# Kernel optimization log

Measured on AMD Instinct MI355X. Metric: run time of the kernel, lower is better.

The kernel has to match this reference:

```python
import jax, jax.numpy as jnp
import numpy as np

B, T, F, U, H = 4096, 64, 128, 256, 256
MC_STEPS = 32
DENOISE = True


def setup_inputs() -> dict:
    key = jax.random.key(0)
    ks = jax.random.split(key, 12)
    su = 1.0 / np.sqrt(U)
    inp = {
        "x": jax.random.normal(ks[0], (B, T, F), jnp.float32),
        # LSTM params (torch gate order i,f,g,o)
        "W_ih": jax.random.uniform(ks[1], (4 * U, F), jnp.float32, -su, su),
        "W_hh": jax.random.uniform(ks[2], (4 * U, U), jnp.float32, -su, su),
        "b_ih": jax.random.uniform(ks[3], (4 * U,), jnp.float32, -su, su),
        "b_hh": jax.random.uniform(ks[4], (4 * U,), jnp.float32, -su, su),
        # CRBM conditioning nets: bias (ny), precision (ny), weights (ny*nh)
        "bias_W": jax.random.normal(ks[5], (F, U), jnp.float32) * su,
        "bias_b": jnp.zeros((F,), jnp.float32),
        "prec_W": jax.random.normal(ks[6], (F, U), jnp.float32) * su,
        "prec_b": jnp.zeros((F,), jnp.float32),
        "wts_W": jax.random.normal(ks[7], (F * H, U), jnp.float32) * su,
        "wts_b": jnp.zeros((F * H,), jnp.float32),
    }
    return inp


def _lstm_last_hidden(x, W_ih, W_hh, b_ih, b_hh):
    # single-layer batch_first LSTM; returns last hidden state [B, U]
    b, u = x.shape[0], W_hh.shape[1]
    bias = b_ih + b_hh

    def step(carry, xt):
        h, c = carry
        g = xt @ W_ih.T + h @ W_hh.T + bias          # [B, 4U]
        i, f, gg, o = jnp.split(g, 4, axis=-1)
        c = jax.nn.sigmoid(f) * c + jax.nn.sigmoid(i) * jnp.tanh(gg)
        h = jax.nn.sigmoid(o) * jnp.tanh(c)
        return (h, c), None

    h0 = jnp.zeros((b, u), x.dtype)
    (h, _), _ = jax.lax.scan(step, (h0, h0), jnp.swapaxes(x, 0, 1))
    return h


def _crbm_sample(xh, bias_W, bias_b, prec_W, prec_b, wts_W, wts_b,
                 mc_steps=MC_STEPS, denoise=DENOISE):
    b = xh.shape[0]
    bias = xh @ bias_W.T + bias_b                              # [B, F]
    precision = jax.nn.softplus(xh @ prec_W.T + prec_b) + 1e-6  # [B, F] > 0
    weights = (xh @ wts_W.T + wts_b).reshape(b, F, H)           # [B, F, H]
    std = jax.lax.rsqrt(precision)

    key = jax.random.key(1)
    k0, kloop = jax.random.split(key)
    y0 = bias + std * jax.random.normal(k0, bias.shape, bias.dtype)

    def gibbs(y, k):
        kh, ky = jax.random.split(k)
        h_prob = jax.nn.sigmoid(jnp.einsum("bf,bfh->bh", y, weights))
        h = (jax.random.uniform(kh, h_prob.shape) < h_prob).astype(y.dtype)
        mean = bias + jnp.einsum("bfh,bh->bf", weights, h) / precision
        y = mean + std * jax.random.normal(ky, mean.shape, mean.dtype)
        return y, mean

    y_last, means = jax.lax.scan(gibbs, y0, jax.random.split(kloop, mc_steps))
    y_model = means[-1] if denoise else y_last
    return y_model, bias, precision, weights


def reference(x, W_ih, W_hh, b_ih, b_hh, bias_W, bias_b, prec_W, prec_b, wts_W, wts_b):
    xh = _lstm_last_hidden(x, W_ih, W_hh, b_ih, b_hh)
    y_model, _, _, _ = _crbm_sample(xh, bias_W, bias_b, prec_W, prec_b, wts_W, wts_b)
    return y_model
```

## Files before the change

kernel.cpp:

```cpp
#include <hip/hip_runtime.h>
#include <stdint.h>

#pragma clang fp contract(off)

#define B 4096
#define T 64
#define F 128
#define U 256
#define H 256
#define GU 1024
#define NJ 32768
#define MC 32
#define CH 256
#define BT 32

__host__ __device__ inline void tf2x32(uint32_t k0, uint32_t k1,
                                       uint32_t x0, uint32_t x1,
                                       uint32_t& o0, uint32_t& o1) {
  uint32_t ks2 = k0 ^ k1 ^ 0x1BD11BDAu;
  x0 += k0; x1 += k1;
#define TFR(r) { x0 += x1; x1 = (x1 << r) | (x1 >> (32 - r)); x1 ^= x0; }
  TFR(13) TFR(15) TFR(26) TFR(6)
  x0 += k1;  x1 += ks2 + 1u;
  TFR(17) TFR(29) TFR(16) TFR(24)
  x0 += ks2; x1 += k0 + 2u;
  TFR(13) TFR(15) TFR(26) TFR(6)
  x0 += k0;  x1 += k1 + 3u;
  TFR(17) TFR(29) TFR(16) TFR(24)
  x0 += k1;  x1 += ks2 + 4u;
  TFR(13) TFR(15) TFR(26) TFR(6)
  x0 += ks2; x1 += k0 + 5u;
#undef TFR
  o0 = x0; o1 = x1;
}

__device__ inline uint32_t tf_bits(uint32_t kx, uint32_t ky, uint32_t i) {
  uint32_t o0, o1;
  tf2x32(kx, ky, 0u, i, o0, o1);
  return o0 ^ o1;
}

__device__ inline float u01_f32(uint32_t bits) {
  return __uint_as_float((bits >> 9) | 0x3F800000u) - 1.0f;
}

__device__ inline float erfinv_f32(float x) {
  float w = -log1pf(-(x * x));
  float p;
  if (w < 5.0f) {
    float ww = w - 2.5f;
    p = 2.81022636e-08f;
    p = p * ww + 3.43273939e-07f;
    p = p * ww + (-3.5233877e-06f);
    p = p * ww + (-4.39150654e-06f);
    p = p * ww + 0.00021858087f;
    p = p * ww + (-0.00125372503f);
    p = p * ww + (-0.00417768164f);
    p = p * ww + 0.246640727f;
    p = p * ww + 1.50140941f;
  } else {
    float ww = sqrtf(w) - 3.0f;
    p = -0.000200214257f;
    p = p * ww + 0.000100950558f;
    p = p * ww + 0.00134934322f;
    p = p * ww + (-0.00367342844f);
    p = p * ww + 0.00573950773f;
    p = p * ww + (-0.0076224613f);
    p = p * ww + 0.00943887047f;
    p = p * ww + 1.00167406f;
    p = p * ww + 2.83297682f;
  }
  return p * x;
}

__device__ inline float normal_f32(uint32_t kx, uint32_t ky, uint32_t i) {
  float f = u01_f32(tf_bits(kx, ky, i));
  const float lo = -0.99999994039535522461f;
  float v = f * 2.0f + lo;
  v = fmaxf(lo, v);
  return 1.4142135623730951f * erfinv_f32(v);
}

__device__ inline float sigmoid_f32(float x) {
  return 1.0f / (1.0f + expf(-x));
}
__device__ inline float softplus_f32(float x) {
  return fmaxf(x, 0.0f) + log1pf(expf(-fabsf(x)));
}

__global__ void prep_lstm_w_k(const float* __restrict__ W_ih, const float* __restrict__ W_hh,
                              const float* __restrict__ b_ih, const float* __restrict__ b_hh,
                              float4* __restrict__ w4t, float* __restrict__ biasg) {
  int idx = blockIdx.x * 256 + threadIdx.x;
  if (idx < GU * 96) {
    int j = idx / 96, k4 = idx - j * 96;
    float v[4];
#pragma unroll
    for (int m = 0; m < 4; ++m) {
      int k = k4 * 4 + m;
      v[m] = (k < F) ? W_ih[(size_t)j * F + k] : W_hh[(size_t)j * U + (k - F)];
    }
    w4t[(size_t)k4 * GU + j] = make_float4(v[0], v[1], v[2], v[3]);
  }
  if (idx < GU) biasg[idx] = b_ih[idx] + b_hh[idx];
}

__global__ void prep_wts_k(const float* __restrict__ wts_W, float4* __restrict__ wts4t) {
  int idx = blockIdx.x * 256 + threadIdx.x;
  if (idx >= NJ * 64) return;
  int j = idx >> 6, k4 = idx & 63;
  const float* r = wts_W + (size_t)j * U + k4 * 4;
  wts4t[(size_t)k4 * NJ + j] = make_float4(r[0], r[1], r[2], r[3]);
}

__global__ void prep_bp_k(const float* __restrict__ bias_W, const float* __restrict__ prec_W,
                          float4* __restrict__ bp4t) {
  int idx = blockIdx.x * 256 + threadIdx.x;
  if (idx >= 256 * 64) return;
  int j = idx >> 6, k4 = idx & 63;
  const float* r = (j < F) ? (bias_W + (size_t)j * U + k4 * 4)
                           : (prec_W + (size_t)(j - F) * U + k4 * 4);
  bp4t[(size_t)k4 * 256 + j] = make_float4(r[0], r[1], r[2], r[3]);
}

__global__ __launch_bounds__(256) void lstm_step_k(
    const float* __restrict__ x, const float* __restrict__ h_in,
    const float* __restrict__ c_in, const float4* __restrict__ w4t,
    const float* __restrict__ biasg, float* __restrict__ h_out,
    float* __restrict__ c_out, int t) {
  __shared__ __align__(16) float xt[BT * 128];
  __shared__ __align__(16) float ht[BT * 256];
  const int tid = threadIdx.x;
  const int b0 = blockIdx.x * BT;
  const int ut = blockIdx.y;
  for (int q = tid; q < BT * 32; q += 256) {
    int row = q >> 5, c4 = q & 31;
    *(float4*)(xt + row * 128 + c4 * 4) =
        *(const float4*)(x + ((size_t)(b0 + row) * T + t) * F + c4 * 4);
  }
  for (int q = tid; q < BT * 64; q += 256) {
    int row = q >> 6, c4 = q & 63;
    *(float4*)(ht + row * 256 + c4 * 4) =
        *(const float4*)(h_in + (size_t)(b0 + row) * U + c4 * 4);
  }
  __syncthreads();
  const int u_loc = tid & 63, bg = tid >> 6;
  const int u = ut * 64 + u_loc;
  float accX[4][8], accH[4][8];
#pragma unroll
  for (int g = 0; g < 4; ++g)
#pragma unroll
    for (int b = 0; b < 8; ++b) { accX[g][b] = 0.0f; accH[g][b] = 0.0f; }

#pragma unroll 4
  for (int k4 = 0; k4 < 32; ++k4) {
    float4 wf[4];
#pragma unroll
    for (int g = 0; g < 4; ++g) wf[g] = w4t[(size_t)k4 * GU + g * U + u];
#pragma unroll
    for (int b = 0; b < 8; ++b) {
      float4 av = *(const float4*)(xt + (bg * 8 + b) * 128 + k4 * 4);
#pragma unroll
      for (int g = 0; g < 4; ++g) {
        accX[g][b] = fmaf(av.x, wf[g].x, accX[g][b]);
        accX[g][b] = fmaf(av.y, wf[g].y, accX[g][b]);
        accX[g][b] = fmaf(av.z, wf[g].z, accX[g][b]);
        accX[g][b] = fmaf(av.w, wf[g].w, accX[g][b]);
      }
    }
  }
#pragma unroll 4
  for (int k4 = 32; k4 < 96; ++k4) {
    float4 wf[4];
#pragma unroll
    for (int g = 0; g < 4; ++g) wf[g] = w4t[(size_t)k4 * GU + g * U + u];
#pragma unroll
    for (int b = 0; b < 8; ++b) {
      float4 av = *(const float4*)(ht + (bg * 8 + b) * 256 + (k4 - 32) * 4);
#pragma unroll
      for (int g = 0; g < 4; ++g) {
        accH[g][b] = fmaf(av.x, wf[g].x, accH[g][b]);
        accH[g][b] = fmaf(av.y, wf[g].y, accH[g][b]);
        accH[g][b] = fmaf(av.z, wf[g].z, accH[g][b]);
        accH[g][b] = fmaf(av.w, wf[g].w, accH[g][b]);
      }
    }
  }
  float bi = biasg[u], bf = biasg[U + u], bgg = biasg[2 * U + u], bo = biasg[3 * U + u];
#pragma unroll
  for (int b = 0; b < 8; ++b) {
    size_t gi = (size_t)(b0 + bg * 8 + b) * U + u;
    float c = c_in[gi];
    float g_i = (accX[0][b] + accH[0][b]) + bi;
    float g_f = (accX[1][b] + accH[1][b]) + bf;
    float g_g = (accX[2][b] + accH[2][b]) + bgg;
    float g_o = (accX[3][b] + accH[3][b]) + bo;
    float t1 = sigmoid_f32(g_f) * c;
    float t2 = sigmoid_f32(g_i) * tanhf(g_g);
    float cn = t1 + t2;
    float hn = sigmoid_f32(g_o) * tanhf(cn);
    c_out[gi] = cn;
    h_out[gi] = hn;
  }
}

__global__ __launch_bounds__(256) void gemm_xh_k(
    const float* __restrict__ xh_c, const float4* __restrict__ wts4t,
    const float* __restrict__ wts_b, float* __restrict__ outp) {
  __shared__ __align__(16) float xl[64 * 256];
  const int tid = threadIdx.x;
  const int b0 = blockIdx.x * 64;
  const int j = blockIdx.y * 256 + tid;
  for (int q = tid; q < 64 * 64; q += 256) {
    int row = q >> 6, c4 = q & 63;
    *(float4*)(xl + row * 256 + c4 * 4) =
        *(const float4*)(xh_c + (size_t)(b0 + row) * U + c4 * 4);
  }
  __syncthreads();
  float acc[64];
#pragma unroll
  for (int b = 0; b < 64; ++b) acc[b] = 0.0f;
  for (int k4 = 0; k4 < 64; ++k4) {
    float4 wf = wts4t[(size_t)k4 * NJ + j];
#pragma unroll
    for (int b = 0; b < 64; ++b) {
      float4 av = *(const float4*)(xl + b * 256 + k4 * 4);
      acc[b] = fmaf(av.x, wf.x, acc[b]);
      acc[b] = fmaf(av.y, wf.y, acc[b]);
      acc[b] = fmaf(av.z, wf.z, acc[b]);
      acc[b] = fmaf(av.w, wf.w, acc[b]);
    }
  }
  float bb = wts_b[j];
#pragma unroll
  for (int b = 0; b < 64; ++b)
    outp[(size_t)(b0 + b) * NJ + j] = acc[b] + bb;
}

__global__ __launch_bounds__(256) void biasprec_k(
    const float* __restrict__ xh, const float4* __restrict__ bp4t,
    const float* __restrict__ bias_b, const float* __restrict__ prec_b,
    float* __restrict__ bias_g, float* __restrict__ prec_g) {
  __shared__ __align__(16) float xl[64 * 256];
  const int tid = threadIdx.x;
  const int b0 = blockIdx.x * 64;
  const int j = tid;
  for (int q = tid; q < 64 * 64; q += 256) {
    int row = q >> 6, c4 = q & 63;
    *(float4*)(xl + row * 256 + c4 * 4) =
        *(const float4*)(xh + (size_t)(b0 + row) * U + c4 * 4);
  }
  __syncthreads();
  float acc[64];
#pragma unroll
  for (int b = 0; b < 64; ++b) acc[b] = 0.0f;
  for (int k4 = 0; k4 < 64; ++k4) {
    float4 wf = bp4t[(size_t)k4 * 256 + j];
#pragma unroll
    for (int b = 0; b < 64; ++b) {
      float4 av = *(const float4*)(xl + b * 256 + k4 * 4);
      acc[b] = fmaf(av.x, wf.x, acc[b]);
      acc[b] = fmaf(av.y, wf.y, acc[b]);
      acc[b] = fmaf(av.z, wf.z, acc[b]);
      acc[b] = fmaf(av.w, wf.w, acc[b]);
    }
  }
  if (j < F) {
    float bb = bias_b[j];
#pragma unroll
    for (int b = 0; b < 64; ++b)
      bias_g[(size_t)(b0 + b) * F + j] = acc[b] + bb;
  } else {
    float pb = prec_b[j - F];
#pragma unroll
    for (int b = 0; b < 64; ++b)
      prec_g[(size_t)(b0 + b) * F + (j - F)] = softplus_f32(acc[b] + pb) + 1e-6f;
  }
}

struct GKeys {
  uint32_t k0x, k0y;
  uint32_t khx[32], khy[32], kyx[32], kyy[32];
};

__global__ __launch_bounds__(256) void gibbs_k(
    const float* __restrict__ w_g, const float* __restrict__ bias_g,
    const float* __restrict__ prec_g, float* __restrict__ outp, GKeys keys,
    int base) {
  __shared__ __align__(16) float wl[32768];
  __shared__ __align__(16) float yv[128];
  __shared__ __align__(16) float hv[256];
  __shared__ float bs[128];
  __shared__ float ps[128];
  __shared__ float ss[128];
  const int tid = threadIdx.x;
  const int bloc = blockIdx.x;
  const int gb = base + bloc;
  const float4* src = (const float4*)(w_g + (size_t)bloc * NJ);
  float4* wl4 = (float4*)wl;
  for (int q = tid; q < NJ / 4; q += 256) {
    int f = q >> 6;
    int j4 = q & 63;
    wl4[f * 64 + (j4 ^ (f & 7))] = src[q];
  }
  if (tid < F) {
    float bb = bias_g[(size_t)gb * F + tid];
    float pp = prec_g[(size_t)gb * F + tid];
    bs[tid] = bb; ps[tid] = pp;
    float sd = 1.0f / sqrtf(pp);
    ss[tid] = sd;
    float n = normal_f32(keys.k0x, keys.k0y, (uint32_t)(gb * F + tid));
    float t1 = sd * n;
    yv[tid] = bb + t1;
  }
  __syncthreads();
  for (int s_ = 0; s_ < MC; ++s_) {
    {
      const int j = tid;
      const int jq = j >> 2, jm = j & 3;
      float u = u01_f32(tf_bits(keys.khx[s_], keys.khy[s_], (uint32_t)(gb * H + j)));
      float acc = 0.0f;
#pragma unroll 4
      for (int fb = 0; fb < F; fb += 4) {
        float4 y4 = *(const float4*)(yv + fb);
        float w0 = wl[(fb + 0) * 256 + ((jq ^ ((fb + 0) & 7)) << 2) + jm];
        float w1 = wl[(fb + 1) * 256 + ((jq ^ ((fb + 1) & 7)) << 2) + jm];
        float w2 = wl[(fb + 2) * 256 + ((jq ^ ((fb + 2) & 7)) << 2) + jm];
        float w3 = wl[(fb + 3) * 256 + ((jq ^ ((fb + 3) & 7)) << 2) + jm];
        acc = fmaf(y4.x, w0, acc);
        acc = fmaf(y4.y, w1, acc);
        acc = fmaf(y4.z, w2, acc);
        acc = fmaf(y4.w, w3, acc);
      }
      float p = sigmoid_f32(acc);
      hv[j] = (u < p) ? 1.0f : 0.0f;
    }
    __syncthreads();
    if (tid < F) {
      const int sq = tid & 7;
      const float4* wr4 = wl4 + tid * 64;
      const float4* hv4 = (const float4*)hv;
      float n = 0.0f;
      if (s_ != MC - 1)
        n = normal_f32(keys.kyx[s_], keys.kyy[s_], (uint32_t)(gb * F + tid));
      float C0[8], C1[8], C2[8], C3[8];
#pragma unroll
      for (int l = 0; l < 8; ++l) { C0[l] = 0.0f; C1[l] = 0.0f; C2[l] = 0.0f; C3[l] = 0.0f; }
      for (int k = 0; k < 8; ++k) {
        int eq = k * 8;
        float4 wq[8], hq[8];
#pragma unroll
        for (int qq = 0; qq < 8; ++qq) {
          wq[qq] = wr4[(eq + qq) ^ sq];
          hq[qq] = hv4[eq + qq];
        }
        const float* wv = (const float*)wq;
        const float* hh = (const float*)hq;
#pragma unroll
        for (int l = 0; l < 8; ++l) {
          C0[l] = fmaf(wv[l],      hh[l],      C0[l]);
          C1[l] = fmaf(wv[8 + l],  hh[8 + l],  C1[l]);
          C2[l] = fmaf(wv[16 + l], hh[16 + l], C2[l]);
          C3[l] = fmaf(wv[24 + l], hh[24 + l], C3[l]);
        }
      }
      float L[8];
#pragma unroll
      for (int l = 0; l < 8; ++l) L[l] = (C0[l] + C1[l]) + (C2[l] + C3[l]);
      float S = ((L[0] + L[1]) + (L[2] + L[3])) + ((L[4] + L[5]) + (L[6] + L[7]));
      float d = S / ps[tid];
      float mean = bs[tid] + d;
      if (s_ == MC - 1) {
        outp[(size_t)gb * F + tid] = mean;
      } else {
        float t1 = ss[tid] * n;
        yv[tid] = mean + t1;
      }
    }
    __syncthreads();
  }
}

extern "C" void kernel_launch(void* const* d_in, const int* in_sizes, int n_in,
                              void* d_out, int out_size, void* d_ws, size_t ws_size,
                              hipStream_t stream) {
  const float* x      = (const float*)d_in[0];
  const float* W_ih   = (const float*)d_in[1];
  const float* W_hh   = (const float*)d_in[2];
  const float* b_ih   = (const float*)d_in[3];
  const float* b_hh   = (const float*)d_in[4];
  const float* bias_W = (const float*)d_in[5];
  const float* bias_b = (const float*)d_in[6];
  const float* prec_W = (const float*)d_in[7];
  const float* prec_b = (const float*)d_in[8];
  const float* wts_W  = (const float*)d_in[9];
  const float* wts_b  = (const float*)d_in[10];
  float* out = (float*)d_out;

  float* wsf = (float*)d_ws;
  size_t off = 0;
  float* w_g     = wsf + off; off += (size_t)CH * NJ;
  float* h_a     = wsf + off; off += (size_t)B * U;
  float* h_b     = wsf + off; off += (size_t)B * U;
  float* c_a     = wsf + off; off += (size_t)B * U;
  float* c_b     = wsf + off; off += (size_t)B * U;
  float* biasg_g = wsf + off; off += (size_t)B * F;
  float* precg_g = wsf + off; off += (size_t)B * F;
  float* w4t     = wsf + off; off += (size_t)96 * GU * 4;
  float* biasg   = wsf + off; off += GU;
  float* wts4t   = wsf + off; off += (size_t)64 * NJ * 4;
  float* bp4t    = wsf + off; off += (size_t)64 * 256 * 4;
  (void)ws_size;

  hipMemsetAsync(h_a, 0, (size_t)B * U * sizeof(float), stream);
  hipMemsetAsync(c_a, 0, (size_t)B * U * sizeof(float), stream);

  prep_lstm_w_k<<<(GU * 96 + 255) / 256, 256, 0, stream>>>(W_ih, W_hh, b_ih, b_hh,
                                                           (float4*)w4t, biasg);
  prep_wts_k<<<(NJ * 64) / 256, 256, 0, stream>>>(wts_W, (float4*)wts4t);
  prep_bp_k<<<(256 * 64) / 256, 256, 0, stream>>>(bias_W, prec_W, (float4*)bp4t);

  const float* hi = h_a; const float* ci = c_a;
  float* ho = h_b; float* co = c_b;
  for (int t = 0; t < T; ++t) {
    lstm_step_k<<<dim3(B / BT, 4), 256, 0, stream>>>(
        x, hi, ci, (const float4*)w4t, biasg, ho, co, t);
    const float* th_ = hi; hi = ho; ho = (float*)th_;
    const float* tc_ = ci; ci = co; co = (float*)tc_;
  }
  const float* xh = hi;

  biasprec_k<<<dim3(B / 64), 256, 0, stream>>>(xh, (const float4*)bp4t,
                                               bias_b, prec_b, biasg_g, precg_g);

  GKeys keys;
  uint32_t k0x, k0y, l0, l1;
  tf2x32(0u, 1u, 0u, 0u, k0x, k0y);
  tf2x32(0u, 1u, 0u, 1u, l0, l1);
  keys.k0x = k0x; keys.k0y = k0y;
  for (int s = 0; s < 32; ++s) {
    uint32_t ksx, ksy;
    tf2x32(l0, l1, 0u, (uint32_t)s, ksx, ksy);
    tf2x32(ksx, ksy, 0u, 0u, keys.khx[s], keys.khy[s]);
    tf2x32(ksx, ksy, 0u, 1u, keys.kyx[s], keys.kyy[s]);
  }

  for (int c = 0; c < B / CH; ++c) {
    gemm_xh_k<<<dim3(CH / 64, NJ / 256), 256, 0, stream>>>(
        xh + (size_t)c * CH * U, (const float4*)wts4t, wts_b, w_g);
    gibbs_k<<<dim3(CH), 256, 0, stream>>>(w_g, biasg_g, precg_g, out, keys, c * CH);
  }
}
```

Baseline: 7.884 ms.

## Retile LSTM, weight-projection and bias/precision GEMM kernels for better register reuse

The LSTM step kernel now computes two hidden-unit columns per thread, so each shared-memory activation load feeds twice as many FMAs, and the grid's unit dimension is halved to match. The weights-projection GEMM switches from 64 accumulators per thread over one output column to an 8x8 register tile (8 columns by 8 batch rows), cutting LDS traffic per FMA. The bias/precision kernel uses 16 batch rows per block instead of 64 to launch more blocks. Together these aim to reduce shared-memory bandwidth pressure and improve occupancy, at the cost of more registers per thread in the LSTM kernel and fewer LSTM blocks per step.

```diff
diff --git a/kernel.cpp b/kernel.cpp
--- a/kernel.cpp
+++ b/kernel.cpp
@@ -132,7 +132,7 @@
   __shared__ __align__(16) float ht[BT * 256];
   const int tid = threadIdx.x;
   const int b0 = blockIdx.x * BT;
-  const int ut = blockIdx.y;
+  const int uh = blockIdx.y;
   for (int q = tid; q < BT * 32; q += 256) {
     int row = q >> 5, c4 = q & 31;
     *(float4*)(xt + row * 128 + c4 * 4) =
@@ -145,62 +145,82 @@
   }
   __syncthreads();
   const int u_loc = tid & 63, bg = tid >> 6;
-  const int u = ut * 64 + u_loc;
-  float accX[4][8], accH[4][8];
+  const int u0 = uh * 128 + u_loc;
+  const int u1 = u0 + 64;
+  float accX[4][8][2], accH[4][8][2];
 #pragma unroll
   for (int g = 0; g < 4; ++g)
 #pragma unroll
-    for (int b = 0; b < 8; ++b) { accX[g][b] = 0.0f; accH[g][b] = 0.0f; }
-
-#pragma unroll 4
+    for (int b = 0; b < 8; ++b) {
+      accX[g][b][0] = 0.0f; accX[g][b][1] = 0.0f;
+      accH[g][b][0] = 0.0f; accH[g][b][1] = 0.0f;
+    }
+
+#pragma unroll 2
   for (int k4 = 0; k4 < 32; ++k4) {
-    float4 wf[4];
-#pragma unroll
-    for (int g = 0; g < 4; ++g) wf[g] = w4t[(size_t)k4 * GU + g * U + u];
+    float4 wf[4][2];
+#pragma unroll
+    for (int g = 0; g < 4; ++g) {
+      wf[g][0] = w4t[(size_t)k4 * GU + g * U + u0];
+      wf[g][1] = w4t[(size_t)k4 * GU + g * U + u1];
+    }
 #pragma unroll
     for (int b = 0; b < 8; ++b) {
       float4 av = *(const float4*)(xt + (bg * 8 + b) * 128 + k4 * 4);
 #pragma unroll
       for (int g = 0; g < 4; ++g) {
-        accX[g][b] = fmaf(av.x, wf[g].x, accX[g][b]);
-        accX[g][b] = fmaf(av.y, wf[g].y, accX[g][b]);
-        accX[g][b] = fmaf(av.z, wf[g].z, accX[g][b]);
-        accX[g][b] = fmaf(av.w, wf[g].w, accX[g][b]);
-      }
-    }
-  }
-#pragma unroll 4
+#pragma unroll
+        for (int s = 0; s < 2; ++s) {
+          accX[g][b][s] = fmaf(av.x, wf[g][s].x, accX[g][b][s]);
+          accX[g][b][s] = fmaf(av.y, wf[g][s].y, accX[g][b][s]);
+          accX[g][b][s] = fmaf(av.z, wf[g][s].z, accX[g][b][s]);
+          accX[g][b][s] = fmaf(av.w, wf[g][s].w, accX[g][b][s]);
+        }
+      }
+    }
+  }
+#pragma unroll 2
   for (int k4 = 32; k4 < 96; ++k4) {
-    float4 wf[4];
-#pragma unroll
-    for (int g = 0; g < 4; ++g) wf[g] = w4t[(size_t)k4 * GU + g * U + u];
+    float4 wf[4][2];
+#pragma unroll
+    for (int g = 0; g < 4; ++g) {
+      wf[g][0] = w4t[(size_t)k4 * GU + g * U + u0];
+      wf[g][1] = w4t[(size_t)k4 * GU + g * U + u1];
+    }
 #pragma unroll
     for (int b = 0; b < 8; ++b) {
       float4 av = *(const float4*)(ht + (bg * 8 + b) * 256 + (k4 - 32) * 4);
 #pragma unroll
       for (int g = 0; g < 4; ++g) {
-        accH[g][b] = fmaf(av.x, wf[g].x, accH[g][b]);
-        accH[g][b] = fmaf(av.y, wf[g].y, accH[g][b]);
-        accH[g][b] = fmaf(av.z, wf[g].z, accH[g][b]);
-        accH[g][b] = fmaf(av.w, wf[g].w, accH[g][b]);
-      }
-    }
-  }
-  float bi = biasg[u], bf = biasg[U + u], bgg = biasg[2 * U + u], bo = biasg[3 * U + u];
-#pragma unroll
-  for (int b = 0; b < 8; ++b) {
-    size_t gi = (size_t)(b0 + bg * 8 + b) * U + u;
-    float c = c_in[gi];
-    float g_i = (accX[0][b] + accH[0][b]) + bi;
-    float g_f = (accX[1][b] + accH[1][b]) + bf;
-    float g_g = (accX[2][b] + accH[2][b]) + bgg;
-    float g_o = (accX[3][b] + accH[3][b]) + bo;
-    float t1 = sigmoid_f32(g_f) * c;
-    float t2 = sigmoid_f32(g_i) * tanhf(g_g);
-    float cn = t1 + t2;
-    float hn = sigmoid_f32(g_o) * tanhf(cn);
-    c_out[gi] = cn;
-    h_out[gi] = hn;
+#pragma unroll
+        for (int s = 0; s < 2; ++s) {
+          accH[g][b][s] = fmaf(av.x, wf[g][s].x, accH[g][b][s]);
+          accH[g][b][s] = fmaf(av.y, wf[g][s].y, accH[g][b][s]);
+          accH[g][b][s] = fmaf(av.z, wf[g][s].z, accH[g][b][s]);
+          accH[g][b][s] = fmaf(av.w, wf[g][s].w, accH[g][b][s]);
+        }
+      }
+    }
+  }
+#pragma unroll
+  for (int s = 0; s < 2; ++s) {
+    int u = (s == 0) ? u0 : u1;
+    float bi = biasg[u], bf = biasg[U + u], bgg = biasg[2 * U + u], bo = biasg[3 * U + u];
+#pragma unroll
+    for (int b = 0; b < 8; ++b) {
+      size_t gi = (size_t)(b0 + bg * 8 + b) * U + u;
+      float c = c_in[gi];
+      float g_i = (accX[0][b][s] + accH[0][b][s]) + bi;
+      float g_f = (accX[1][b][s] + accH[1][b][s]) + bf;
+      float g_g = (accX[2][b][s] + accH[2][b][s]) + bgg;
+      float g_o = (accX[3][b][s] + accH[3][b][s]) + bo;
+      float t1 = sigmoid_f32(g_f) * c;
+      float t2 = sigmoid_f32(g_i) * tanhf(g_g);
+      float cn = t1 + t2;
+      float hn = sigmoid_f32(g_o) * tanhf(cn);
+      c_out[gi] = cn;
+      h_out[gi] = hn;
+    }
   }
 }
 
@@ -210,20 +230,68 @@
   __shared__ __align__(16) float xl[64 * 256];
   const int tid = threadIdx.x;
   const int b0 = blockIdx.x * 64;
-  const int j = blockIdx.y * 256 + tid;
+  const int jb = blockIdx.y * 256;
+  const int jl = tid & 31, bg = tid >> 5;
   for (int q = tid; q < 64 * 64; q += 256) {
     int row = q >> 6, c4 = q & 63;
     *(float4*)(xl + row * 256 + c4 * 4) =
         *(const float4*)(xh_c + (size_t)(b0 + row) * U + c4 * 4);
   }
   __syncthreads();
-  float acc[64];
-#pragma unroll
-  for (int b = 0; b < 64; ++b) acc[b] = 0.0f;
+  float acc[8][8];
+#pragma unroll
+  for (int q = 0; q < 8; ++q)
+#pragma unroll
+    for (int bb = 0; bb < 8; ++bb) acc[q][bb] = 0.0f;
+#pragma unroll 2
   for (int k4 = 0; k4 < 64; ++k4) {
-    float4 wf = wts4t[(size_t)k4 * NJ + j];
-#pragma unroll
-    for (int b = 0; b < 64; ++b) {
+    float4 wf[8];
+#pragma unroll
+    for (int q = 0; q < 8; ++q)
+      wf[q] = wts4t[(size_t)k4 * NJ + jb + q * 32 + jl];
+#pragma unroll
+    for (int bb = 0; bb < 8; ++bb) {
+      float4 av = *(const float4*)(xl + (bg * 8 + bb) * 256 + k4 * 4);
+#pragma unroll
+      for (int q = 0; q < 8; ++q) {
+        acc[q][bb] = fmaf(av.x, wf[q].x, acc[q][bb]);
+        acc[q][bb] = fmaf(av.y, wf[q].y, acc[q][bb]);
+        acc[q][bb] = fmaf(av.z, wf[q].z, acc[q][bb]);
+        acc[q][bb] = fmaf(av.w, wf[q].w, acc[q][bb]);
+      }
+    }
+  }
+#pragma unroll
+  for (int q = 0; q < 8; ++q) {
+    float bb_j = wts_b[jb + q * 32 + jl];
+#pragma unroll
+    for (int bb = 0; bb < 8; ++bb)
+      outp[(size_t)(b0 + bg * 8 + bb) * NJ + jb + q * 32 + jl] = acc[q][bb] + bb_j;
+  }
+}
+
+__global__ __launch_bounds__(256) void biasprec_k(
+    const float* __restrict__ xh, const float4* __restrict__ bp4t,
+    const float* __restrict__ bias_b, const float* __restrict__ prec_b,
+    float* __restrict__ bias_g, float* __restrict__ prec_g) {
+  __shared__ __align__(16) float xl[16 * 256];
+  const int tid = threadIdx.x;
+  const int b0 = blockIdx.x * 16;
+  const int j = tid;
+  for (int q = tid; q < 16 * 64; q += 256) {
+    int row = q >> 6, c4 = q & 63;
+    *(float4*)(xl + row * 256 + c4 * 4) =
+        *(const float4*)(xh + (size_t)(b0 + row) * U + c4 * 4);
+  }
+  __syncthreads();
+  float acc[16];
+#pragma unroll
+  for (int b = 0; b < 16; ++b) acc[b] = 0.0f;
+#pragma unroll 2
+  for (int k4 = 0; k4 < 64; ++k4) {
+    float4 wf = bp4t[(size_t)k4 * 256 + j];
+#pragma unroll
+    for (int b = 0; b < 16; ++b) {
       float4 av = *(const float4*)(xl + b * 256 + k4 * 4);
       acc[b] = fmaf(av.x, wf.x, acc[b]);
       acc[b] = fmaf(av.y, wf.y, acc[b]);
@@ -231,49 +299,15 @@
       acc[b] = fmaf(av.w, wf.w, acc[b]);
     }
   }
-  float bb = wts_b[j];
-#pragma unroll
-  for (int b = 0; b < 64; ++b)
-    outp[(size_t)(b0 + b) * NJ + j] = acc[b] + bb;
-}
-
-__global__ __launch_bounds__(256) void biasprec_k(
-    const float* __restrict__ xh, const float4* __restrict__ bp4t,
-    const float* __restrict__ bias_b, const float* __restrict__ prec_b,
-    float* __restrict__ bias_g, float* __restrict__ prec_g) {
-  __shared__ __align__(16) float xl[64 * 256];
-  const int tid = threadIdx.x;
-  const int b0 = blockIdx.x * 64;
-  const int j = tid;
-  for (int q = tid; q < 64 * 64; q += 256) {
-    int row = q >> 6, c4 = q & 63;
-    *(float4*)(xl + row * 256 + c4 * 4) =
-        *(const float4*)(xh + (size_t)(b0 + row) * U + c4 * 4);
-  }
-  __syncthreads();
-  float acc[64];
-#pragma unroll
-  for (int b = 0; b < 64; ++b) acc[b] = 0.0f;
-  for (int k4 = 0; k4 < 64; ++k4) {
-    float4 wf = bp4t[(size_t)k4 * 256 + j];
-#pragma unroll
-    for (int b = 0; b < 64; ++b) {
-      float4 av = *(const float4*)(xl + b * 256 + k4 * 4);
-      acc[b] = fmaf(av.x, wf.x, acc[b]);
-      acc[b] = fmaf(av.y, wf.y, acc[b]);
-      acc[b] = fmaf(av.z, wf.z, acc[b]);
-      acc[b] = fmaf(av.w, wf.w, acc[b]);
-    }
-  }
   if (j < F) {
     float bb = bias_b[j];
 #pragma unroll
-    for (int b = 0; b < 64; ++b)
+    for (int b = 0; b < 16; ++b)
       bias_g[(size_t)(b0 + b) * F + j] = acc[b] + bb;
   } else {
     float pb = prec_b[j - F];
 #pragma unroll
-    for (int b = 0; b < 64; ++b)
+    for (int b = 0; b < 16; ++b)
       prec_g[(size_t)(b0 + b) * F + (j - F)] = softplus_f32(acc[b] + pb) + 1e-6f;
   }
 }
@@ -423,14 +457,14 @@
   const float* hi = h_a; const float* ci = c_a;
   float* ho = h_b; float* co = c_b;
   for (int t = 0; t < T; ++t) {
-    lstm_step_k<<<dim3(B / BT, 4), 256, 0, stream>>>(
+    lstm_step_k<<<dim3(B / BT, 2), 256, 0, stream>>>(
         x, hi, ci, (const float4*)w4t, biasg, ho, co, t);
     const float* th_ = hi; hi = ho; ho = (float*)th_;
     const float* tc_ = ci; ci = co; co = (float*)tc_;
   }
   const float* xh = hi;
 
-  biasprec_k<<<dim3(B / 64), 256, 0, stream>>>(xh, (const float4*)bp4t,
+  biasprec_k<<<dim3(B / 16), 256, 0, stream>>>(xh, (const float4*)bp4t,
                                                bias_b, prec_b, biasg_g, precg_g);
 
   GKeys keys;
```

Measured after the change: 6.991 ms. -11.3%, faster.
